# Kernel tuning notes

Measured on AMD Instinct MI355X. Metric: run time of the kernel, lower is better.

The kernel has to match this reference:

```python
import jax, jax.numpy as jnp
import numpy as np
import math

B, T, D = 2, 2048, 4096
H, HD = 32, 128  # n_head, head_dim; H*HD == D
THETA = 10000.0


def _rope_tables(T, hd, theta):
    # standard RoPE: freqs_i = theta^(-2i/hd), angle[t,i] = t * freqs_i
    inv = 1.0 / (theta ** (np.arange(0, hd, 2, dtype=np.float32) / hd))  # [hd/2]
    ang = np.arange(T, dtype=np.float32)[:, None] * inv[None, :]          # [T, hd/2]
    return jnp.asarray(np.cos(ang)), jnp.asarray(np.sin(ang))


def setup_inputs() -> dict:
    key = jax.random.key(0)
    ks = jax.random.split(key, 5)
    scale = 1.0 / math.sqrt(D)
    x = jax.random.normal(ks[0], (B, T, D), dtype=jnp.float32)
    Wq = jax.random.normal(ks[1], (D, H * HD), dtype=jnp.float32) * scale
    Wk = jax.random.normal(ks[2], (D, H * HD), dtype=jnp.float32) * scale
    Wv = jax.random.normal(ks[3], (D, H * HD), dtype=jnp.float32) * scale
    Wo = jax.random.normal(ks[4], (D, D), dtype=jnp.float32) * scale
    fc, fs = _rope_tables(T, HD, THETA)
    return {"x": x, "freqs_cos": fc, "freqs_sin": fs,
            "Wq": Wq, "Wk": Wk, "Wv": Wv, "Wo": Wo}


def _apply_rope(t, cos, sin):
    # t: [B, T, H, HD]; complex rotation on interleaved (even, odd) pairs
    tp = t.reshape(*t.shape[:-1], HD // 2, 2)
    xr, xi = tp[..., 0], tp[..., 1]
    c = cos[None, :, None, :]  # [1, T, 1, HD/2]
    s = sin[None, :, None, :]
    out_r = xr * c - xi * s
    out_i = xr * s + xi * c
    return jnp.stack([out_r, out_i], axis=-1).reshape(t.shape)


def reference(x, freqs_cos, freqs_sin, Wq, Wk, Wv, Wo):
    Bc, Tc, _ = x.shape
    q = (x @ Wq).reshape(Bc, Tc, H, HD)
    k = (x @ Wk).reshape(Bc, Tc, H, HD)
    v = (x @ Wv).reshape(Bc, Tc, H, HD)
    q = _apply_rope(q, freqs_cos, freqs_sin)
    k = _apply_rope(k, freqs_cos, freqs_sin)
    scale = 1.0 / math.sqrt(HD)
    scores = jnp.einsum('bqhd,bkhd->bhqk', q, k) * scale  # [B,H,T,T]
    causal = jnp.tril(jnp.ones((Tc, Tc), dtype=bool))
    scores = jnp.where(causal[None, None], scores, -jnp.inf)
    attn = jax.nn.softmax(scores, axis=-1)
    y = jnp.einsum('bhqk,bkhd->bqhd', attn, v).reshape(Bc, Tc, H * HD)
    return y @ Wo
```

## Files before the change

kernel.cpp:

```cpp
#include <hip/hip_runtime.h>

typedef unsigned short ushort_t;
typedef unsigned int uint32;

typedef float f32x4 __attribute__((ext_vector_type(4)));
typedef __bf16 bf16x8 __attribute__((ext_vector_type(8)));
typedef unsigned short us8 __attribute__((ext_vector_type(8)));
typedef unsigned short us4 __attribute__((ext_vector_type(4)));

#define TSEQ 2048
#define DMODEL 4096

__device__ __forceinline__ ushort_t f2bf(float f) {
  uint32 u = __builtin_bit_cast(uint32, f);
  u += 0x7FFFu + ((u >> 16) & 1u);
  return (ushort_t)(u >> 16);
}
__device__ __forceinline__ float bf2f(ushort_t u) {
  return __builtin_bit_cast(float, ((uint32)u) << 16);
}

__device__ __forceinline__ void gload_lds16(const void* g, void* l) {
  auto gp = (const __attribute__((address_space(1))) void*)g;
  auto lp = (__attribute__((address_space(3))) void*)l;
  __builtin_amdgcn_global_load_lds(gp, lp, 16, 0, 0);
}

__global__ __launch_bounds__(256) void k_cast_bf16(const float* __restrict__ in,
                                                   ushort_t* __restrict__ out, int n4) {
  int g = blockIdx.x * 256 + threadIdx.x;
  if (g >= n4) return;
  float4 v = *(const float4*)(in + (size_t)g * 4);
  us4 o; o[0] = f2bf(v.x); o[1] = f2bf(v.y); o[2] = f2bf(v.z); o[3] = f2bf(v.w);
  *(us4*)(out + (size_t)g * 4) = o;
}

__global__ __launch_bounds__(256) void k_transpose_cast4(const float* __restrict__ W0,
                                                         const float* __restrict__ W1,
                                                         const float* __restrict__ W2,
                                                         const float* __restrict__ W3,
                                                         ushort_t* __restrict__ WTbase) {
  __shared__ __align__(16) ushort_t ts[64 * 72];
  const float* Ws[4] = {W0, W1, W2, W3};
  const float* W = Ws[blockIdx.z];
  ushort_t* WT = WTbase + (size_t)blockIdx.z * DMODEL * DMODEL;
  const int tid = threadIdx.x;
  const int n0 = blockIdx.x * 64, k0 = blockIdx.y * 64;
  #pragma unroll
  for (int it = 0; it < 4; ++it) {
    int e = it * 256 + tid;
    int r = e >> 4, c4 = e & 15;
    float4 v = *(const float4*)(W + (size_t)(k0 + r) * DMODEL + n0 + c4 * 4);
    us4 o; o[0] = f2bf(v.x); o[1] = f2bf(v.y); o[2] = f2bf(v.z); o[3] = f2bf(v.w);
    *(us4*)&ts[r * 72 + c4 * 4] = o;
  }
  __syncthreads();
  #pragma unroll
  for (int it = 0; it < 4; ++it) {
    int e = it * 256 + tid;
    int r2 = e >> 4, c4 = e & 15;
    us4 o;
    #pragma unroll
    for (int j = 0; j < 4; ++j) o[j] = ts[(c4 * 4 + j) * 72 + r2];
    *(us4*)(WT + (size_t)(n0 + r2) * DMODEL + k0 + c4 * 4) = o;
  }
}

template <bool OUT_BF16, bool ROPE>
__global__ __launch_bounds__(512, 2)
void k_gemm256(const ushort_t* __restrict__ A, const ushort_t* __restrict__ Bt,
               void* __restrict__ Cv, int M, int N, int K,
               const float* __restrict__ fc, const float* __restrict__ fs) {
  __shared__ __align__(16) ushort_t As[2][256 * 64];
  __shared__ __align__(16) ushort_t Bs[2][256 * 64];
  const int tid = threadIdx.x;
  const int w = tid >> 6, l = tid & 63;
  const int wr = w >> 2, wc = w & 3;
  const int lg = l >> 4, lc = l & 15;

  const int nwg = gridDim.x;
  const int cpx = nwg >> 3;
  const int wg = (blockIdx.x & 7) * cpx + (blockIdx.x >> 3);
  const int nbn = N >> 8;
  const int bm = wg / nbn, bn = wg % nbn;

  const int rowoff = l >> 3;
  const int swzck  = (l & 7) ^ rowoff;
  const ushort_t* Ab = A + (size_t)(bm * 256) * K;
  const ushort_t* Bb = Bt + (size_t)(bn * 256) * K;
  const ushort_t* gA[4]; const ushort_t* gB[4];
  int ldsOff[4];
  #pragma unroll
  for (int j = 0; j < 4; ++j) {
    int r0 = (w * 4 + j) * 8;
    gA[j] = Ab + (size_t)(r0 + rowoff) * K + swzck * 8;
    gB[j] = Bb + (size_t)(r0 + rowoff) * K + swzck * 8;
    ldsOff[j] = r0 * 64;
  }

  int offA[8][2], offB[4][2];
  #pragma unroll
  for (int m = 0; m < 8; ++m)
    #pragma unroll
    for (int kk = 0; kk < 2; ++kk)
      offA[m][kk] = (wr * 128 + m * 16 + lc) * 64 + (((kk * 4 + lg) ^ (lc & 7)) * 8);
  #pragma unroll
  for (int n = 0; n < 4; ++n)
    #pragma unroll
    for (int kk = 0; kk < 2; ++kk)
      offB[n][kk] = (wc * 64 + n * 16 + lc) * 64 + (((kk * 4 + lg) ^ (lc & 7)) * 8);

  f32x4 acc[8][4];
  #pragma unroll
  for (int m = 0; m < 8; ++m)
    #pragma unroll
    for (int n = 0; n < 4; ++n) acc[m][n] = (f32x4){0.f, 0.f, 0.f, 0.f};

  #pragma unroll
  for (int j = 0; j < 4; ++j) {
    gload_lds16(gA[j], &As[0][ldsOff[j]]);
    gload_lds16(gB[j], &Bs[0][ldsOff[j]]);
  }
  #pragma unroll
  for (int j = 0; j < 4; ++j) {
    gload_lds16(gA[j] + 64, &As[1][ldsOff[j]]);
    gload_lds16(gB[j] + 64, &Bs[1][ldsOff[j]]);
  }
  asm volatile("s_waitcnt vmcnt(8)" ::: "memory");
  __builtin_amdgcn_s_barrier();
  __builtin_amdgcn_sched_barrier(0);

  const int NT = K >> 6;
  for (int t = 0; t < NT; ++t) {
    const int cur = t & 1;
    const ushort_t* Ac = As[cur];
    const ushort_t* Bc = Bs[cur];
    bf16x8 af[4][2], b0[2][2], b1[2][2];

    #pragma unroll
    for (int i = 0; i < 4; ++i)
      #pragma unroll
      for (int kk = 0; kk < 2; ++kk)
        af[i][kk] = *(const bf16x8*)&Ac[offA[i][kk]];
    #pragma unroll
    for (int j2 = 0; j2 < 2; ++j2)
      #pragma unroll
      for (int kk = 0; kk < 2; ++kk) {
        b0[j2][kk] = *(const bf16x8*)&Bc[offB[j2][kk]];
        b1[j2][kk] = *(const bf16x8*)&Bc[offB[2 + j2][kk]];
      }
    asm volatile("" ::: "memory");
    __builtin_amdgcn_s_barrier();

    __builtin_amdgcn_s_setprio(1);
    #pragma unroll
    for (int i = 0; i < 4; ++i)
      #pragma unroll
      for (int j2 = 0; j2 < 2; ++j2)
        #pragma unroll
        for (int kk = 0; kk < 2; ++kk) {
          acc[i][j2]     = __builtin_amdgcn_mfma_f32_16x16x32_bf16(af[i][kk], b0[j2][kk], acc[i][j2], 0, 0, 0);
          acc[i][2 + j2] = __builtin_amdgcn_mfma_f32_16x16x32_bf16(af[i][kk], b1[j2][kk], acc[i][2 + j2], 0, 0, 0);
        }
    __builtin_amdgcn_s_setprio(0);

    #pragma unroll
    for (int i = 0; i < 4; ++i)
      #pragma unroll
      for (int kk = 0; kk < 2; ++kk)
        af[i][kk] = *(const bf16x8*)&Ac[offA[4 + i][kk]];
    asm volatile("" ::: "memory");
    __builtin_amdgcn_s_barrier();

    __builtin_amdgcn_s_setprio(1);
    #pragma unroll
    for (int i = 0; i < 4; ++i)
      #pragma unroll
      for (int j2 = 0; j2 < 2; ++j2)
        #pragma unroll
        for (int kk = 0; kk < 2; ++kk) {
          acc[4 + i][j2]     = __builtin_amdgcn_mfma_f32_16x16x32_bf16(af[i][kk], b0[j2][kk], acc[4 + i][j2], 0, 0, 0);
          acc[4 + i][2 + j2] = __builtin_amdgcn_mfma_f32_16x16x32_bf16(af[i][kk], b1[j2][kk], acc[4 + i][2 + j2], 0, 0, 0);
        }
    __builtin_amdgcn_s_setprio(0);
    asm volatile("" ::: "memory");
    __builtin_amdgcn_s_barrier();

    if (t + 2 < NT) {
      const int k0 = (t + 2) << 6;
      #pragma unroll
      for (int j = 0; j < 4; ++j) {
        gload_lds16(gA[j] + k0, &As[cur][ldsOff[j]]);
        gload_lds16(gB[j] + k0, &Bs[cur][ldsOff[j]]);
      }
      asm volatile("s_waitcnt vmcnt(8)" ::: "memory");
    } else if (t + 1 < NT) {
      asm volatile("s_waitcnt vmcnt(0)" ::: "memory");
    }
    if (t + 1 < NT) {
      __builtin_amdgcn_s_barrier();
      __builtin_amdgcn_sched_barrier(0);
    }
  }

  #pragma unroll
  for (int m = 0; m < 8; ++m) {
    int row0 = bm * 256 + wr * 128 + m * 16 + lg * 4;
    #pragma unroll
    for (int n = 0; n < 4; ++n) {
      int col = bn * 256 + wc * 64 + n * 16 + lc;
      if (ROPE) {
        int i0 = (col & 127) >> 1;
        #pragma unroll
        for (int r = 0; r < 4; ++r) {
          int tt = (row0 + r) & (TSEQ - 1);
          float c = fc[tt * 64 + i0];
          float s = fs[tt * 64 + i0];
          float v = acc[m][n][r];
          float p = __shfl_xor(v, 1);
          float ov = (lc & 1) ? (p * s + v * c) : (v * c - p * s);
          ((ushort_t*)Cv)[(size_t)(row0 + r) * N + col] = f2bf(ov);
        }
      } else {
        #pragma unroll
        for (int r = 0; r < 4; ++r) {
          float v = acc[m][n][r];
          if (OUT_BF16) ((ushort_t*)Cv)[(size_t)(row0 + r) * N + col] = f2bf(v);
          else          ((float*)Cv)[(size_t)(row0 + r) * N + col] = v;
        }
      }
    }
  }
}

__global__ __launch_bounds__(512, 2)
void k_attn(const ushort_t* __restrict__ Q, const ushort_t* __restrict__ Kb,
            const ushort_t* __restrict__ Vt, ushort_t* __restrict__ Y) {
  __shared__ __align__(16) ushort_t Ks[2][64 * 128];
  __shared__ __align__(16) ushort_t Vs[2][128 * 64];
  __shared__ __align__(16) ushort_t Ps[8][16 * 64];
  const int id = blockIdx.x;
  const int xcd = id & 7, slot = id >> 3;
  const int bx = slot & 7, gHi = slot >> 3;
  const int g = gHi * 8 + xcd;
  const int h = g & 31, b = g >> 5;
  const int tid = threadIdx.x;
  const int w = tid >> 6, l = tid & 63;
  const int lg = l >> 4, lc = l & 15;
  const float scale = 0.08838834764831845f;
  const float THR = 8.0f;

  auto stageKV = [&](int kv0, int buf) {
    #pragma unroll
    for (int i = 0; i < 2; ++i) {
      int seg = w * 2 + i;
      {
        int row = seg * 4 + (l >> 4);
        int csrc = (l & 15) ^ (row & 7);
        gload_lds16(Kb + (size_t)(b * TSEQ + kv0 + row) * DMODEL + h * 128 + csrc * 8,
                    &Ks[buf][seg * 512]);
      }
      {
        int row = seg * 8 + (l >> 3);
        int csrc = (l & 7) ^ (l >> 3);
        gload_lds16(Vt + (size_t)(h * 128 + row) * DMODEL + b * TSEQ + kv0 + csrc * 8,
                    &Vs[buf][seg * 512]);
      }
    }
  };

  for (int qi = 0; qi < 2; ++qi) {
    const int qt = qi ? (15 - bx) : bx;
    const int q0 = qt * 128;
    const int wrow0 = q0 + w * 16;

    bf16x8 qf[4];
    {
      const ushort_t* qp = Q + (size_t)(b * TSEQ + wrow0 + lc) * DMODEL + h * 128;
      #pragma unroll
      for (int ks = 0; ks < 4; ++ks) qf[ks] = *(const bf16x8*)(qp + ks * 32 + lg * 8);
    }

    float m_r[4], lp[4];
    #pragma unroll
    for (int r = 0; r < 4; ++r) { m_r[r] = -1e30f; lp[r] = 0.f; }
    f32x4 o[8];
    #pragma unroll
    for (int t = 0; t < 8; ++t) o[t] = (f32x4){0.f, 0.f, 0.f, 0.f};

    const int nkv = (qt + 1) * 2;
    stageKV(0, 0);
    for (int kt = 0; kt < nkv; ++kt) {
      const int cur = kt & 1;
      const int kv0 = kt * 64;
      if (kt + 1 < nkv) {
        stageKV((kt + 1) * 64, cur ^ 1);
        asm volatile("s_waitcnt vmcnt(4)" ::: "memory");
      } else {
        asm volatile("s_waitcnt vmcnt(0)" ::: "memory");
      }
      __builtin_amdgcn_s_barrier();

      if (kv0 <= wrow0 + 15) {
        f32x4 s[4];
        __builtin_amdgcn_s_setprio(1);
        #pragma unroll
        for (int n = 0; n < 4; ++n) {
          s[n] = (f32x4){0.f, 0.f, 0.f, 0.f};
          #pragma unroll
          for (int ks = 0; ks < 4; ++ks) {
            int row = n * 16 + lc;
            bf16x8 kf = *(const bf16x8*)&Ks[cur][row * 128 + ((ks * 32 + lg * 8) ^ ((row & 7) * 8))];
            s[n] = __builtin_amdgcn_mfma_f32_16x16x32_bf16(qf[ks], kf, s[n], 0, 0, 0);
          }
        }
        __builtin_amdgcn_s_setprio(0);

        float sv[4][4];
        if (kv0 + 63 > wrow0) {
          #pragma unroll
          for (int n = 0; n < 4; ++n)
            #pragma unroll
            for (int r = 0; r < 4; ++r) {
              float x = s[n][r] * scale;
              int kvg = kv0 + n * 16 + lc;
              int qg = wrow0 + lg * 4 + r;
              sv[n][r] = (kvg > qg) ? -1e30f : x;
            }
        } else {
          #pragma unroll
          for (int n = 0; n < 4; ++n)
            #pragma unroll
            for (int r = 0; r < 4; ++r) sv[n][r] = s[n][r] * scale;
        }

        float pmax[4];
        #pragma unroll
        for (int r = 0; r < 4; ++r)
          pmax[r] = fmaxf(fmaxf(sv[0][r], sv[1][r]), fmaxf(sv[2][r], sv[3][r]));
        bool ok = (pmax[0] <= m_r[0] + THR) && (pmax[1] <= m_r[1] + THR) &&
                  (pmax[2] <= m_r[2] + THR) && (pmax[3] <= m_r[3] + THR);
        if (!__all(ok)) {
          #pragma unroll
          for (int r = 0; r < 4; ++r) {
            float mx = pmax[r];
            #pragma unroll
            for (int off = 1; off < 16; off <<= 1) mx = fmaxf(mx, __shfl_xor(mx, off, 16));
            float mn = fmaxf(m_r[r], mx);
            float al = __expf(m_r[r] - mn);
            m_r[r] = mn;
            lp[r] *= al;
            #pragma unroll
            for (int t = 0; t < 8; ++t) o[t][r] *= al;
          }
        }

        #pragma unroll
        for (int n = 0; n < 4; ++n)
          #pragma unroll
          for (int r = 0; r < 4; ++r) {
            float p = __expf(sv[n][r] - m_r[r]);
            lp[r] += p;
            int row = lg * 4 + r, col = n * 16 + lc;
            Ps[w][row * 64 + (col ^ (lg * 16))] = f2bf(p);
          }

        __builtin_amdgcn_s_setprio(1);
        #pragma unroll
        for (int kvs = 0; kvs < 2; ++kvs) {
          bf16x8 pa = *(const bf16x8*)&Ps[w][lc * 64 + ((kvs * 32 + lg * 8) ^ ((lc >> 2) * 16))];
          #pragma unroll
          for (int t = 0; t < 8; ++t) {
            int vrow = t * 16 + lc;
            bf16x8 vb = *(const bf16x8*)&Vs[cur][vrow * 64 + ((kvs * 32 + lg * 8) ^ ((vrow & 7) * 8))];
            o[t] = __builtin_amdgcn_mfma_f32_16x16x32_bf16(pa, vb, o[t], 0, 0, 0);
          }
        }
        __builtin_amdgcn_s_setprio(0);
      }
      asm volatile("" ::: "memory");
      __builtin_amdgcn_s_barrier();
    }

    float linv[4];
    #pragma unroll
    for (int r = 0; r < 4; ++r) {
      float ls = lp[r];
      #pragma unroll
      for (int off = 1; off < 16; off <<= 1) ls += __shfl_xor(ls, off, 16);
      linv[r] = 1.0f / ls;
    }

    #pragma unroll
    for (int t = 0; t < 8; ++t)
      #pragma unroll
      for (int r = 0; r < 4; ++r) {
        int row = wrow0 + lg * 4 + r;
        int col = h * 128 + t * 16 + lc;
        Y[(size_t)(b * TSEQ + row) * DMODEL + col] = f2bf(o[t][r] * linv[r]);
      }
  }
}

extern "C" void kernel_launch(void* const* d_in, const int* in_sizes, int n_in,
                              void* d_out, int out_size, void* d_ws, size_t ws_size,
                              hipStream_t stream) {
  const float* x  = (const float*)d_in[0];
  const float* fc = (const float*)d_in[1];
  const float* fs = (const float*)d_in[2];
  const float* Wq = (const float*)d_in[3];
  const float* Wk = (const float*)d_in[4];
  const float* Wv = (const float*)d_in[5];
  const float* Wo = (const float*)d_in[6];

  const size_t SZ = (size_t)4096 * 4096;
  ushort_t* xb  = (ushort_t*)d_ws;
  ushort_t* WqT = xb + SZ;
  ushort_t* WkT = WqT + SZ;
  ushort_t* WvT = WkT + SZ;
  ushort_t* WoT = WvT + SZ;
  ushort_t* qb  = WoT + SZ;
  ushort_t* kb  = qb + SZ;
  ushort_t* vT  = kb + SZ;
  ushort_t* yb  = vT + SZ;

  k_cast_bf16<<<16384, 256, 0, stream>>>(x, xb, 4194304);
  dim3 tg(64, 64, 4);
  k_transpose_cast4<<<tg, 256, 0, stream>>>(Wq, Wk, Wv, Wo, WqT);

  k_gemm256<true, true><<<256, 512, 0, stream>>>(xb, WqT, qb, 4096, 4096, 4096, fc, fs);
  k_gemm256<true, true><<<256, 512, 0, stream>>>(xb, WkT, kb, 4096, 4096, 4096, fc, fs);
  k_gemm256<true, false><<<256, 512, 0, stream>>>(WvT, xb, vT, 4096, 4096, 4096, nullptr, nullptr);

  k_attn<<<512, 512, 0, stream>>>(qb, kb, vT, yb);

  k_gemm256<false, false><<<256, 512, 0, stream>>>(yb, WoT, d_out, 4096, 4096, 4096, nullptr, nullptr);
}
```

Baseline: 902.5 us.

## Interleave global-to-LDS prefetch into quarter-tile MFMA phases of GEMM loop

Restructures the 256x256 GEMM main loop so each K-tile runs as four MFMA quadrants. Each quadrant is preceded by issuing a slice of the next tile's global-to-LDS loads into regions already consumed, instead of issuing all prefetches at the end of the tile. The goal is to spread memory traffic across the compute phases and overlap it more finely with MFMA work. The cost is more barriers per tile and tighter vmcnt/lgkmcnt bookkeeping. Loads past the last tile are clamped to tile NT-1, so a few redundant loads are issued at the tail.

```diff
diff --git a/kernel.cpp b/kernel.cpp
--- a/kernel.cpp
+++ b/kernel.cpp
@@ -84,19 +84,20 @@
   const int nbn = N >> 8;
   const int bm = wg / nbn, bn = wg % nbn;
 
-  const int rowoff = l >> 3;
-  const int swzck  = (l & 7) ^ rowoff;
   const ushort_t* Ab = A + (size_t)(bm * 256) * K;
   const ushort_t* Bb = Bt + (size_t)(bn * 256) * K;
-  const ushort_t* gA[4]; const ushort_t* gB[4];
-  int ldsOff[4];
-  #pragma unroll
-  for (int j = 0; j < 4; ++j) {
-    int r0 = (w * 4 + j) * 8;
-    gA[j] = Ab + (size_t)(r0 + rowoff) * K + swzck * 8;
-    gB[j] = Bb + (size_t)(r0 + rowoff) * K + swzck * 8;
-    ldsOff[j] = r0 * 64;
-  }
+
+  int aS0[2], aS1[2], bS0[2], bS1[2];
+  #pragma unroll
+  for (int j = 0; j < 2; ++j) {
+    aS0[j] = (w < 4) ? (2 * w + j) : (8 + 2 * w + j);
+    aS1[j] = aS0[j] + 8;
+    int i2 = 2 * w + j;
+    bS0[j] = (i2 >> 2) * 8 + (i2 & 3);
+    bS1[j] = bS0[j] + 4;
+  }
+  const int rowoff = l >> 3;
+  const int swz = (l & 7) ^ rowoff;
 
   int offA[8][2], offB[4][2];
   #pragma unroll
@@ -116,27 +117,25 @@
     #pragma unroll
     for (int n = 0; n < 4; ++n) acc[m][n] = (f32x4){0.f, 0.f, 0.f, 0.f};
 
-  #pragma unroll
-  for (int j = 0; j < 4; ++j) {
-    gload_lds16(gA[j], &As[0][ldsOff[j]]);
-    gload_lds16(gB[j], &Bs[0][ldsOff[j]]);
-  }
-  #pragma unroll
-  for (int j = 0; j < 4; ++j) {
-    gload_lds16(gA[j] + 64, &As[1][ldsOff[j]]);
-    gload_lds16(gB[j] + 64, &Bs[1][ldsOff[j]]);
-  }
-  asm volatile("s_waitcnt vmcnt(8)" ::: "memory");
+  const int NT = K >> 6;
+  auto stg = [&](const ushort_t* gb, ushort_t* lds, int s, int tl) {
+    int k0 = ((tl < NT) ? tl : (NT - 1)) << 6;
+    gload_lds16(gb + (size_t)(s * 8 + rowoff) * K + k0 + swz * 8, lds + s * 512);
+  };
+
+  stg(Ab, As[0], aS0[0], 0); stg(Ab, As[0], aS0[1], 0);
+  stg(Bb, Bs[0], bS0[0], 0); stg(Bb, Bs[0], bS0[1], 0);
+  stg(Bb, Bs[0], bS1[0], 0); stg(Bb, Bs[0], bS1[1], 0);
+  stg(Ab, As[0], aS1[0], 0); stg(Ab, As[0], aS1[1], 0);
+  stg(Ab, As[1], aS0[0], 1); stg(Ab, As[1], aS0[1], 1);
+  stg(Bb, Bs[1], bS0[0], 1); stg(Bb, Bs[1], bS0[1], 1);
+  stg(Bb, Bs[1], bS1[0], 1); stg(Bb, Bs[1], bS1[1], 1);
+  asm volatile("s_waitcnt vmcnt(6)" ::: "memory");
   __builtin_amdgcn_s_barrier();
-  __builtin_amdgcn_sched_barrier(0);
-
-  const int NT = K >> 6;
-  for (int t = 0; t < NT; ++t) {
-    const int cur = t & 1;
-    const ushort_t* Ac = As[cur];
-    const ushort_t* Bc = Bs[cur];
-    bf16x8 af[4][2], b0[2][2], b1[2][2];
-
+
+  auto pass = [&](const ushort_t* Ac, const ushort_t* Bc, ushort_t* AsOth,
+                  ushort_t* AsCur, ushort_t* BsCur, int tA1, int tM) {
+    bf16x8 af[4][2], b0r[2][2], b1r[2][2];
     #pragma unroll
     for (int i = 0; i < 4; ++i)
       #pragma unroll
@@ -145,62 +144,85 @@
     #pragma unroll
     for (int j2 = 0; j2 < 2; ++j2)
       #pragma unroll
-      for (int kk = 0; kk < 2; ++kk) {
-        b0[j2][kk] = *(const bf16x8*)&Bc[offB[j2][kk]];
-        b1[j2][kk] = *(const bf16x8*)&Bc[offB[2 + j2][kk]];
-      }
+      for (int kk = 0; kk < 2; ++kk)
+        b0r[j2][kk] = *(const bf16x8*)&Bc[offB[j2][kk]];
+    stg(Ab, AsOth, aS1[0], tA1); stg(Ab, AsOth, aS1[1], tA1);
+    asm volatile("s_waitcnt lgkmcnt(8)" ::: "memory");
+    __builtin_amdgcn_s_barrier();
+    asm volatile("s_waitcnt lgkmcnt(0)" ::: "memory");
+    __builtin_amdgcn_sched_barrier(0);
+    __builtin_amdgcn_s_setprio(1);
+    #pragma unroll
+    for (int i = 0; i < 4; ++i)
+      #pragma unroll
+      for (int j2 = 0; j2 < 2; ++j2)
+        #pragma unroll
+        for (int kk = 0; kk < 2; ++kk)
+          acc[i][j2] = __builtin_amdgcn_mfma_f32_16x16x32_bf16(af[i][kk], b0r[j2][kk], acc[i][j2], 0, 0, 0);
+    __builtin_amdgcn_s_setprio(0);
+    __builtin_amdgcn_s_barrier();
+
+    #pragma unroll
+    for (int j2 = 0; j2 < 2; ++j2)
+      #pragma unroll
+      for (int kk = 0; kk < 2; ++kk)
+        b1r[j2][kk] = *(const bf16x8*)&Bc[offB[2 + j2][kk]];
+    stg(Ab, AsCur, aS0[0], tM); stg(Ab, AsCur, aS0[1], tM);
     asm volatile("" ::: "memory");
     __builtin_amdgcn_s_barrier();
-
+    asm volatile("s_waitcnt lgkmcnt(0)" ::: "memory");
+    __builtin_amdgcn_sched_barrier(0);
     __builtin_amdgcn_s_setprio(1);
     #pragma unroll
     for (int i = 0; i < 4; ++i)
       #pragma unroll
       for (int j2 = 0; j2 < 2; ++j2)
         #pragma unroll
-        for (int kk = 0; kk < 2; ++kk) {
-          acc[i][j2]     = __builtin_amdgcn_mfma_f32_16x16x32_bf16(af[i][kk], b0[j2][kk], acc[i][j2], 0, 0, 0);
-          acc[i][2 + j2] = __builtin_amdgcn_mfma_f32_16x16x32_bf16(af[i][kk], b1[j2][kk], acc[i][2 + j2], 0, 0, 0);
-        }
+        for (int kk = 0; kk < 2; ++kk)
+          acc[i][2 + j2] = __builtin_amdgcn_mfma_f32_16x16x32_bf16(af[i][kk], b1r[j2][kk], acc[i][2 + j2], 0, 0, 0);
     __builtin_amdgcn_s_setprio(0);
+    __builtin_amdgcn_s_barrier();
 
     #pragma unroll
     for (int i = 0; i < 4; ++i)
       #pragma unroll
       for (int kk = 0; kk < 2; ++kk)
         af[i][kk] = *(const bf16x8*)&Ac[offA[4 + i][kk]];
+    stg(Bb, BsCur, bS0[0], tM); stg(Bb, BsCur, bS0[1], tM);
     asm volatile("" ::: "memory");
     __builtin_amdgcn_s_barrier();
-
+    asm volatile("s_waitcnt lgkmcnt(0)" ::: "memory");
+    __builtin_amdgcn_sched_barrier(0);
     __builtin_amdgcn_s_setprio(1);
     #pragma unroll
     for (int i = 0; i < 4; ++i)
       #pragma unroll
       for (int j2 = 0; j2 < 2; ++j2)
         #pragma unroll
-        for (int kk = 0; kk < 2; ++kk) {
-          acc[4 + i][j2]     = __builtin_amdgcn_mfma_f32_16x16x32_bf16(af[i][kk], b0[j2][kk], acc[4 + i][j2], 0, 0, 0);
-          acc[4 + i][2 + j2] = __builtin_amdgcn_mfma_f32_16x16x32_bf16(af[i][kk], b1[j2][kk], acc[4 + i][2 + j2], 0, 0, 0);
-        }
+        for (int kk = 0; kk < 2; ++kk)
+          acc[4 + i][2 + j2] = __builtin_amdgcn_mfma_f32_16x16x32_bf16(af[i][kk], b1r[j2][kk], acc[4 + i][2 + j2], 0, 0, 0);
     __builtin_amdgcn_s_setprio(0);
+    __builtin_amdgcn_s_barrier();
+
+    stg(Bb, BsCur, bS1[0], tM); stg(Bb, BsCur, bS1[1], tM);
     asm volatile("" ::: "memory");
     __builtin_amdgcn_s_barrier();
-
-    if (t + 2 < NT) {
-      const int k0 = (t + 2) << 6;
-      #pragma unroll
-      for (int j = 0; j < 4; ++j) {
-        gload_lds16(gA[j] + k0, &As[cur][ldsOff[j]]);
-        gload_lds16(gB[j] + k0, &Bs[cur][ldsOff[j]]);
-      }
-      asm volatile("s_waitcnt vmcnt(8)" ::: "memory");
-    } else if (t + 1 < NT) {
-      asm volatile("s_waitcnt vmcnt(0)" ::: "memory");
-    }
-    if (t + 1 < NT) {
-      __builtin_amdgcn_s_barrier();
-      __builtin_amdgcn_sched_barrier(0);
-    }
+    __builtin_amdgcn_s_setprio(1);
+    #pragma unroll
+    for (int i = 0; i < 4; ++i)
+      #pragma unroll
+      for (int j2 = 0; j2 < 2; ++j2)
+        #pragma unroll
+        for (int kk = 0; kk < 2; ++kk)
+          acc[4 + i][j2] = __builtin_amdgcn_mfma_f32_16x16x32_bf16(af[i][kk], b0r[j2][kk], acc[4 + i][j2], 0, 0, 0);
+    __builtin_amdgcn_s_setprio(0);
+    asm volatile("s_waitcnt vmcnt(6)" ::: "memory");
+    __builtin_amdgcn_s_barrier();
+  };
+
+  for (int t2 = 0; t2 < NT; t2 += 2) {
+    pass(As[0], Bs[0], As[1], As[0], Bs[0], t2 + 1, t2 + 2);
+    pass(As[1], Bs[1], As[0], As[1], Bs[1], t2 + 2, t2 + 3);
   }
 
   #pragma unroll
```

After: 859.4 us. 1.05x faster.

## Fuse Q and K projections into one wide GEMM; add 32x32 MFMA GEMM for V

Applied to the files above, without the earlier changes.

Runs the Q and K projections as one N=8192 GEMM launch with 512 blocks, writing an interleaved QK buffer with row stride 8192 that the attention kernel now reads. This relies on WqT and WkT being contiguous so they form a single transposed weight. A new k_gemm32 kernel using 32x32x16 MFMA computes the V projection. The main GEMM's inner loop is also split into four barrier-separated MFMA phases, so B-fragment loads and the next global prefetch interleave with compute. The aim is to cut launch count, fill the GPU better and raise MFMA efficiency, at the cost of extra barriers per iteration.

```diff
diff --git a/kernel.cpp b/kernel.cpp
--- a/kernel.cpp
+++ b/kernel.cpp
@@ -4,6 +4,7 @@
 typedef unsigned int uint32;
 
 typedef float f32x4 __attribute__((ext_vector_type(4)));
+typedef float f32x16 __attribute__((ext_vector_type(16)));
 typedef __bf16 bf16x8 __attribute__((ext_vector_type(8)));
 typedef unsigned short us8 __attribute__((ext_vector_type(8)));
 typedef unsigned short us4 __attribute__((ext_vector_type(4)));
@@ -135,7 +136,7 @@
     const int cur = t & 1;
     const ushort_t* Ac = As[cur];
     const ushort_t* Bc = Bs[cur];
-    bf16x8 af[4][2], b0[2][2], b1[2][2];
+    bf16x8 af[4][2], bf0[2][2], bf1[2][2];
 
     #pragma unroll
     for (int i = 0; i < 4; ++i)
@@ -145,24 +146,40 @@
     #pragma unroll
     for (int j2 = 0; j2 < 2; ++j2)
       #pragma unroll
-      for (int kk = 0; kk < 2; ++kk) {
-        b0[j2][kk] = *(const bf16x8*)&Bc[offB[j2][kk]];
-        b1[j2][kk] = *(const bf16x8*)&Bc[offB[2 + j2][kk]];
-      }
-    asm volatile("" ::: "memory");
-    __builtin_amdgcn_s_barrier();
-
+      for (int kk = 0; kk < 2; ++kk)
+        bf0[j2][kk] = *(const bf16x8*)&Bc[offB[j2][kk]];
+    asm volatile("" ::: "memory");
+    __builtin_amdgcn_s_barrier();
     __builtin_amdgcn_s_setprio(1);
     #pragma unroll
     for (int i = 0; i < 4; ++i)
       #pragma unroll
       for (int j2 = 0; j2 < 2; ++j2)
         #pragma unroll
-        for (int kk = 0; kk < 2; ++kk) {
-          acc[i][j2]     = __builtin_amdgcn_mfma_f32_16x16x32_bf16(af[i][kk], b0[j2][kk], acc[i][j2], 0, 0, 0);
-          acc[i][2 + j2] = __builtin_amdgcn_mfma_f32_16x16x32_bf16(af[i][kk], b1[j2][kk], acc[i][2 + j2], 0, 0, 0);
-        }
-    __builtin_amdgcn_s_setprio(0);
+        for (int kk = 0; kk < 2; ++kk)
+          acc[i][j2] = __builtin_amdgcn_mfma_f32_16x16x32_bf16(af[i][kk], bf0[j2][kk], acc[i][j2], 0, 0, 0);
+    __builtin_amdgcn_s_setprio(0);
+    __builtin_amdgcn_s_barrier();
+    asm volatile("" ::: "memory");
+
+    #pragma unroll
+    for (int j2 = 0; j2 < 2; ++j2)
+      #pragma unroll
+      for (int kk = 0; kk < 2; ++kk)
+        bf1[j2][kk] = *(const bf16x8*)&Bc[offB[2 + j2][kk]];
+    asm volatile("" ::: "memory");
+    __builtin_amdgcn_s_barrier();
+    __builtin_amdgcn_s_setprio(1);
+    #pragma unroll
+    for (int i = 0; i < 4; ++i)
+      #pragma unroll
+      for (int j2 = 0; j2 < 2; ++j2)
+        #pragma unroll
+        for (int kk = 0; kk < 2; ++kk)
+          acc[i][2 + j2] = __builtin_amdgcn_mfma_f32_16x16x32_bf16(af[i][kk], bf1[j2][kk], acc[i][2 + j2], 0, 0, 0);
+    __builtin_amdgcn_s_setprio(0);
+    __builtin_amdgcn_s_barrier();
+    asm volatile("" ::: "memory");
 
     #pragma unroll
     for (int i = 0; i < 4; ++i)
@@ -171,20 +188,17 @@
         af[i][kk] = *(const bf16x8*)&Ac[offA[4 + i][kk]];
     asm volatile("" ::: "memory");
     __builtin_amdgcn_s_barrier();
-
     __builtin_amdgcn_s_setprio(1);
     #pragma unroll
     for (int i = 0; i < 4; ++i)
       #pragma unroll
       for (int j2 = 0; j2 < 2; ++j2)
         #pragma unroll
-        for (int kk = 0; kk < 2; ++kk) {
-          acc[4 + i][j2]     = __builtin_amdgcn_mfma_f32_16x16x32_bf16(af[i][kk], b0[j2][kk], acc[4 + i][j2], 0, 0, 0);
-          acc[4 + i][2 + j2] = __builtin_amdgcn_mfma_f32_16x16x32_bf16(af[i][kk], b1[j2][kk], acc[4 + i][2 + j2], 0, 0, 0);
-        }
-    __builtin_amdgcn_s_setprio(0);
-    asm volatile("" ::: "memory");
-    __builtin_amdgcn_s_barrier();
+        for (int kk = 0; kk < 2; ++kk)
+          acc[4 + i][j2] = __builtin_amdgcn_mfma_f32_16x16x32_bf16(af[i][kk], bf0[j2][kk], acc[4 + i][j2], 0, 0, 0);
+    __builtin_amdgcn_s_setprio(0);
+    __builtin_amdgcn_s_barrier();
+    asm volatile("" ::: "memory");
 
     if (t + 2 < NT) {
       const int k0 = (t + 2) << 6;
@@ -193,6 +207,20 @@
         gload_lds16(gA[j] + k0, &As[cur][ldsOff[j]]);
         gload_lds16(gB[j] + k0, &Bs[cur][ldsOff[j]]);
       }
+    }
+    asm volatile("" ::: "memory");
+    __builtin_amdgcn_s_barrier();
+    __builtin_amdgcn_s_setprio(1);
+    #pragma unroll
+    for (int i = 0; i < 4; ++i)
+      #pragma unroll
+      for (int j2 = 0; j2 < 2; ++j2)
+        #pragma unroll
+        for (int kk = 0; kk < 2; ++kk)
+          acc[4 + i][2 + j2] = __builtin_amdgcn_mfma_f32_16x16x32_bf16(af[i][kk], bf1[j2][kk], acc[4 + i][2 + j2], 0, 0, 0);
+    __builtin_amdgcn_s_setprio(0);
+
+    if (t + 2 < NT) {
       asm volatile("s_waitcnt vmcnt(8)" ::: "memory");
     } else if (t + 1 < NT) {
       asm volatile("s_waitcnt vmcnt(0)" ::: "memory");
@@ -234,8 +262,174 @@
 }
 
 __global__ __launch_bounds__(512, 2)
-void k_attn(const ushort_t* __restrict__ Q, const ushort_t* __restrict__ Kb,
-            const ushort_t* __restrict__ Vt, ushort_t* __restrict__ Y) {
+void k_gemm32(const ushort_t* __restrict__ A, const ushort_t* __restrict__ Bt,
+              ushort_t* __restrict__ C, int M, int N, int K) {
+  __shared__ __align__(16) ushort_t As[2][256 * 64];
+  __shared__ __align__(16) ushort_t Bs[2][256 * 64];
+  const int tid = threadIdx.x;
+  const int w = tid >> 6, l = tid & 63;
+  const int wr = w >> 2, wc = w & 3;
+  const int lh = l >> 5, ll = l & 31;
+
+  const int nwg = gridDim.x;
+  const int cpx = nwg >> 3;
+  const int wg = (blockIdx.x & 7) * cpx + (blockIdx.x >> 3);
+  const int nbn = N >> 8;
+  const int bm = wg / nbn, bn = wg % nbn;
+
+  const int rowoff = l >> 3;
+  const int swzck  = (l & 7) ^ rowoff;
+  const ushort_t* Ab = A + (size_t)(bm * 256) * K;
+  const ushort_t* Bb = Bt + (size_t)(bn * 256) * K;
+  const ushort_t* gA[4]; const ushort_t* gB[4];
+  int ldsOff[4];
+  #pragma unroll
+  for (int j = 0; j < 4; ++j) {
+    int r0 = (w * 4 + j) * 8;
+    gA[j] = Ab + (size_t)(r0 + rowoff) * K + swzck * 8;
+    gB[j] = Bb + (size_t)(r0 + rowoff) * K + swzck * 8;
+    ldsOff[j] = r0 * 64;
+  }
+
+  int offA[4][4], offB[2][4];
+  #pragma unroll
+  for (int m = 0; m < 4; ++m)
+    #pragma unroll
+    for (int ks = 0; ks < 4; ++ks)
+      offA[m][ks] = (wr * 128 + m * 32 + ll) * 64 + (((ks * 2 + lh) ^ (ll & 7)) * 8);
+  #pragma unroll
+  for (int n = 0; n < 2; ++n)
+    #pragma unroll
+    for (int ks = 0; ks < 4; ++ks)
+      offB[n][ks] = (wc * 64 + n * 32 + ll) * 64 + (((ks * 2 + lh) ^ (ll & 7)) * 8);
+
+  f32x16 acc[4][2];
+  #pragma unroll
+  for (int m = 0; m < 4; ++m)
+    #pragma unroll
+    for (int n = 0; n < 2; ++n)
+      #pragma unroll
+      for (int r = 0; r < 16; ++r) acc[m][n][r] = 0.f;
+
+  #pragma unroll
+  for (int j = 0; j < 4; ++j) {
+    gload_lds16(gA[j], &As[0][ldsOff[j]]);
+    gload_lds16(gB[j], &Bs[0][ldsOff[j]]);
+  }
+  #pragma unroll
+  for (int j = 0; j < 4; ++j) {
+    gload_lds16(gA[j] + 64, &As[1][ldsOff[j]]);
+    gload_lds16(gB[j] + 64, &Bs[1][ldsOff[j]]);
+  }
+  asm volatile("s_waitcnt vmcnt(8)" ::: "memory");
+  __builtin_amdgcn_s_barrier();
+  __builtin_amdgcn_sched_barrier(0);
+
+  const int NT = K >> 6;
+  for (int t = 0; t < NT; ++t) {
+    const int cur = t & 1;
+    const ushort_t* Ac = As[cur];
+    const ushort_t* Bc = Bs[cur];
+    bf16x8 af[2][4], bf0[4], bf1[4];
+
+    #pragma unroll
+    for (int i = 0; i < 2; ++i)
+      #pragma unroll
+      for (int ks = 0; ks < 4; ++ks)
+        af[i][ks] = *(const bf16x8*)&Ac[offA[i][ks]];
+    #pragma unroll
+    for (int ks = 0; ks < 4; ++ks)
+      bf0[ks] = *(const bf16x8*)&Bc[offB[0][ks]];
+    asm volatile("" ::: "memory");
+    __builtin_amdgcn_s_barrier();
+    __builtin_amdgcn_s_setprio(1);
+    #pragma unroll
+    for (int i = 0; i < 2; ++i)
+      #pragma unroll
+      for (int ks = 0; ks < 4; ++ks)
+        acc[i][0] = __builtin_amdgcn_mfma_f32_32x32x16_bf16(af[i][ks], bf0[ks], acc[i][0], 0, 0, 0);
+    __builtin_amdgcn_s_setprio(0);
+    __builtin_amdgcn_s_barrier();
+    asm volatile("" ::: "memory");
+
+    #pragma unroll
+    for (int ks = 0; ks < 4; ++ks)
+      bf1[ks] = *(const bf16x8*)&Bc[offB[1][ks]];
+    asm volatile("" ::: "memory");
+    __builtin_amdgcn_s_barrier();
+    __builtin_amdgcn_s_setprio(1);
+    #pragma unroll
+    for (int i = 0; i < 2; ++i)
+      #pragma unroll
+      for (int ks = 0; ks < 4; ++ks)
+        acc[i][1] = __builtin_amdgcn_mfma_f32_32x32x16_bf16(af[i][ks], bf1[ks], acc[i][1], 0, 0, 0);
+    __builtin_amdgcn_s_setprio(0);
+    __builtin_amdgcn_s_barrier();
+    asm volatile("" ::: "memory");
+
+    #pragma unroll
+    for (int i = 0; i < 2; ++i)
+      #pragma unroll
+      for (int ks = 0; ks < 4; ++ks)
+        af[i][ks] = *(const bf16x8*)&Ac[offA[2 + i][ks]];
+    asm volatile("" ::: "memory");
+    __builtin_amdgcn_s_barrier();
+    __builtin_amdgcn_s_setprio(1);
+    #pragma unroll
+    for (int i = 0; i < 2; ++i)
+      #pragma unroll
+      for (int ks = 0; ks < 4; ++ks)
+        acc[2 + i][0] = __builtin_amdgcn_mfma_f32_32x32x16_bf16(af[i][ks], bf0[ks], acc[2 + i][0], 0, 0, 0);
+    __builtin_amdgcn_s_setprio(0);
+    __builtin_amdgcn_s_barrier();
+    asm volatile("" ::: "memory");
+
+    if (t + 2 < NT) {
+      const int k0 = (t + 2) << 6;
+      #pragma unroll
+      for (int j = 0; j < 4; ++j) {
+        gload_lds16(gA[j] + k0, &As[cur][ldsOff[j]]);
+        gload_lds16(gB[j] + k0, &Bs[cur][ldsOff[j]]);
+      }
+    }
+    asm volatile("" ::: "memory");
+    __builtin_amdgcn_s_barrier();
+    __builtin_amdgcn_s_setprio(1);
+    #pragma unroll
+    for (int i = 0; i < 2; ++i)
+      #pragma unroll
+      for (int ks = 0; ks < 4; ++ks)
+        acc[2 + i][1] = __builtin_amdgcn_mfma_f32_32x32x16_bf16(af[i][ks], bf1[ks], acc[2 + i][1], 0, 0, 0);
+    __builtin_amdgcn_s_setprio(0);
+
+    if (t + 2 < NT) {
+      asm volatile("s_waitcnt vmcnt(8)" ::: "memory");
+    } else if (t + 1 < NT) {
+      asm volatile("s_waitcnt vmcnt(0)" ::: "memory");
+    }
+    if (t + 1 < NT) {
+      __builtin_amdgcn_s_barrier();
+      __builtin_amdgcn_sched_barrier(0);
+    }
+  }
+
+  #pragma unroll
+  for (int m = 0; m < 4; ++m) {
+    #pragma unroll
+    for (int n = 0; n < 2; ++n) {
+      int col = bn * 256 + wc * 64 + n * 32 + ll;
+      #pragma unroll
+      for (int r = 0; r < 16; ++r) {
+        int row = bm * 256 + wr * 128 + m * 32 + (r & 3) + 8 * (r >> 2) + 4 * lh;
+        C[(size_t)row * N + col] = f2bf(acc[m][n][r]);
+      }
+    }
+  }
+}
+
+__global__ __launch_bounds__(512, 2)
+void k_attn(const ushort_t* __restrict__ QK, const ushort_t* __restrict__ Vt,
+            ushort_t* __restrict__ Y) {
   __shared__ __align__(16) ushort_t Ks[2][64 * 128];
   __shared__ __align__(16) ushort_t Vs[2][128 * 64];
   __shared__ __align__(16) ushort_t Ps[8][16 * 64];
@@ -249,6 +443,7 @@
   const int lg = l >> 4, lc = l & 15;
   const float scale = 0.08838834764831845f;
   const float THR = 8.0f;
+  const int QKS = 8192;
 
   auto stageKV = [&](int kv0, int buf) {
     #pragma unroll
@@ -257,7 +452,7 @@
       {
         int row = seg * 4 + (l >> 4);
         int csrc = (l & 15) ^ (row & 7);
-        gload_lds16(Kb + (size_t)(b * TSEQ + kv0 + row) * DMODEL + h * 128 + csrc * 8,
+        gload_lds16(QK + (size_t)(b * TSEQ + kv0 + row) * QKS + 4096 + h * 128 + csrc * 8,
                     &Ks[buf][seg * 512]);
       }
       {
@@ -276,7 +471,7 @@
 
     bf16x8 qf[4];
     {
-      const ushort_t* qp = Q + (size_t)(b * TSEQ + wrow0 + lc) * DMODEL + h * 128;
+      const ushort_t* qp = QK + (size_t)(b * TSEQ + wrow0 + lc) * QKS + h * 128;
       #pragma unroll
       for (int ks = 0; ks < 4; ++ks) qf[ks] = *(const bf16x8*)(qp + ks * 32 + lg * 8);
     }
@@ -419,20 +614,18 @@
   ushort_t* WkT = WqT + SZ;
   ushort_t* WvT = WkT + SZ;
   ushort_t* WoT = WvT + SZ;
-  ushort_t* qb  = WoT + SZ;
-  ushort_t* kb  = qb + SZ;
-  ushort_t* vT  = kb + SZ;
+  ushort_t* qk  = WoT + SZ;
+  ushort_t* vT  = qk + 2 * SZ;
   ushort_t* yb  = vT + SZ;
 
   k_cast_bf16<<<16384, 256, 0, stream>>>(x, xb, 4194304);
   dim3 tg(64, 64, 4);
   k_transpose_cast4<<<tg, 256, 0, stream>>>(Wq, Wk, Wv, Wo, WqT);
 
-  k_gemm256<true, true><<<256, 512, 0, stream>>>(xb, WqT, qb, 4096, 4096, 4096, fc, fs);
-  k_gemm256<true, true><<<256, 512, 0, stream>>>(xb, WkT, kb, 4096, 4096, 4096, fc, fs);
-  k_gemm256<true, false><<<256, 512, 0, stream>>>(WvT, xb, vT, 4096, 4096, 4096, nullptr, nullptr);
-
-  k_attn<<<512, 512, 0, stream>>>(qb, kb, vT, yb);
+  k_gemm256<true, true><<<512, 512, 0, stream>>>(xb, WqT, qk, 4096, 8192, 4096, fc, fs);
+  k_gemm32<<<256, 512, 0, stream>>>(WvT, xb, vT, 4096, 4096, 4096);
+
+  k_attn<<<512, 512, 0, stream>>>(qk, vT, yb);
 
   k_gemm256<false, false><<<256, 512, 0, stream>>>(yb, WoT, d_out, 4096, 4096, 4096, nullptr, nullptr);
 }
```

Measured after the change: 901.9 us. Within noise of the previous version (-0.1%).

## Split GEMM main loop into four MFMA phases, overlapping prefetch with last phase

Applied to the files above, without the earlier changes.

Restructures the inner K-loop of the bf16 GEMM into four quadrant phases, each with its own LDS fragment loads and barriers. B fragments are loaded in two halves, and the global-to-LDS prefetch for tile t+2 is issued before the final MFMA quadrant so it overlaps compute. The intent is to hide global load latency and interleave LDS reads with MFMA work, in a ping-pong style schedule. The cost is extra barriers per iteration and a more intricate ordering that could add stalls.

```diff
diff --git a/kernel.cpp b/kernel.cpp
--- a/kernel.cpp
+++ b/kernel.cpp
@@ -135,7 +135,7 @@
     const int cur = t & 1;
     const ushort_t* Ac = As[cur];
     const ushort_t* Bc = Bs[cur];
-    bf16x8 af[4][2], b0[2][2], b1[2][2];
+    bf16x8 af[4][2], bf0[2][2], bf1[2][2];
 
     #pragma unroll
     for (int i = 0; i < 4; ++i)
@@ -145,24 +145,40 @@
     #pragma unroll
     for (int j2 = 0; j2 < 2; ++j2)
       #pragma unroll
-      for (int kk = 0; kk < 2; ++kk) {
-        b0[j2][kk] = *(const bf16x8*)&Bc[offB[j2][kk]];
-        b1[j2][kk] = *(const bf16x8*)&Bc[offB[2 + j2][kk]];
-      }
-    asm volatile("" ::: "memory");
-    __builtin_amdgcn_s_barrier();
-
+      for (int kk = 0; kk < 2; ++kk)
+        bf0[j2][kk] = *(const bf16x8*)&Bc[offB[j2][kk]];
+    asm volatile("" ::: "memory");
+    __builtin_amdgcn_s_barrier();
     __builtin_amdgcn_s_setprio(1);
     #pragma unroll
     for (int i = 0; i < 4; ++i)
       #pragma unroll
       for (int j2 = 0; j2 < 2; ++j2)
         #pragma unroll
-        for (int kk = 0; kk < 2; ++kk) {
-          acc[i][j2]     = __builtin_amdgcn_mfma_f32_16x16x32_bf16(af[i][kk], b0[j2][kk], acc[i][j2], 0, 0, 0);
-          acc[i][2 + j2] = __builtin_amdgcn_mfma_f32_16x16x32_bf16(af[i][kk], b1[j2][kk], acc[i][2 + j2], 0, 0, 0);
-        }
+        for (int kk = 0; kk < 2; ++kk)
+          acc[i][j2] = __builtin_amdgcn_mfma_f32_16x16x32_bf16(af[i][kk], bf0[j2][kk], acc[i][j2], 0, 0, 0);
     __builtin_amdgcn_s_setprio(0);
+    __builtin_amdgcn_s_barrier();
+    asm volatile("" ::: "memory");
+
+    #pragma unroll
+    for (int j2 = 0; j2 < 2; ++j2)
+      #pragma unroll
+      for (int kk = 0; kk < 2; ++kk)
+        bf1[j2][kk] = *(const bf16x8*)&Bc[offB[2 + j2][kk]];
+    asm volatile("" ::: "memory");
+    __builtin_amdgcn_s_barrier();
+    __builtin_amdgcn_s_setprio(1);
+    #pragma unroll
+    for (int i = 0; i < 4; ++i)
+      #pragma unroll
+      for (int j2 = 0; j2 < 2; ++j2)
+        #pragma unroll
+        for (int kk = 0; kk < 2; ++kk)
+          acc[i][2 + j2] = __builtin_amdgcn_mfma_f32_16x16x32_bf16(af[i][kk], bf1[j2][kk], acc[i][2 + j2], 0, 0, 0);
+    __builtin_amdgcn_s_setprio(0);
+    __builtin_amdgcn_s_barrier();
+    asm volatile("" ::: "memory");
 
     #pragma unroll
     for (int i = 0; i < 4; ++i)
@@ -171,20 +187,17 @@
         af[i][kk] = *(const bf16x8*)&Ac[offA[4 + i][kk]];
     asm volatile("" ::: "memory");
     __builtin_amdgcn_s_barrier();
-
     __builtin_amdgcn_s_setprio(1);
     #pragma unroll
     for (int i = 0; i < 4; ++i)
       #pragma unroll
       for (int j2 = 0; j2 < 2; ++j2)
         #pragma unroll
-        for (int kk = 0; kk < 2; ++kk) {
-          acc[4 + i][j2]     = __builtin_amdgcn_mfma_f32_16x16x32_bf16(af[i][kk], b0[j2][kk], acc[4 + i][j2], 0, 0, 0);
-          acc[4 + i][2 + j2] = __builtin_amdgcn_mfma_f32_16x16x32_bf16(af[i][kk], b1[j2][kk], acc[4 + i][2 + j2], 0, 0, 0);
-        }
+        for (int kk = 0; kk < 2; ++kk)
+          acc[4 + i][j2] = __builtin_amdgcn_mfma_f32_16x16x32_bf16(af[i][kk], bf0[j2][kk], acc[4 + i][j2], 0, 0, 0);
     __builtin_amdgcn_s_setprio(0);
-    asm volatile("" ::: "memory");
-    __builtin_amdgcn_s_barrier();
+    __builtin_amdgcn_s_barrier();
+    asm volatile("" ::: "memory");
 
     if (t + 2 < NT) {
       const int k0 = (t + 2) << 6;
@@ -193,6 +206,20 @@
         gload_lds16(gA[j] + k0, &As[cur][ldsOff[j]]);
         gload_lds16(gB[j] + k0, &Bs[cur][ldsOff[j]]);
       }
+    }
+    asm volatile("" ::: "memory");
+    __builtin_amdgcn_s_barrier();
+    __builtin_amdgcn_s_setprio(1);
+    #pragma unroll
+    for (int i = 0; i < 4; ++i)
+      #pragma unroll
+      for (int j2 = 0; j2 < 2; ++j2)
+        #pragma unroll
+        for (int kk = 0; kk < 2; ++kk)
+          acc[4 + i][2 + j2] = __builtin_amdgcn_mfma_f32_16x16x32_bf16(af[i][kk], bf1[j2][kk], acc[4 + i][2 + j2], 0, 0, 0);
+    __builtin_amdgcn_s_setprio(0);
+
+    if (t + 2 < NT) {
       asm volatile("s_waitcnt vmcnt(8)" ::: "memory");
     } else if (t + 1 < NT) {
       asm volatile("s_waitcnt vmcnt(0)" ::: "memory");
```

Result: faster. 863.9 us (-4.3%).
